# Kernel optimization log

Measured on AMD Instinct MI355X. Metric: run time of the kernel, lower is better.

## Reference

```python
import jax, jax.numpy as jnp
import numpy as np

STATE_DIM = 2
HIDDEN = 1024
N_SKILLS = 5
N_ACTIONS = 4
BATCH = 65536


def setup_inputs() -> dict:
    key = jax.random.key(0)
    ks = jax.random.split(key, 8)
    def lin_init(k, fan_in, shape):
        bound = 1.0 / np.sqrt(fan_in)
        return jax.random.uniform(k, shape, jnp.float32, -bound, bound)
    return {
        "s": jax.random.normal(ks[0], (BATCH, STATE_DIM), jnp.float32),
        "skill_idx": jax.random.randint(ks[1], (BATCH,), 0, N_SKILLS, jnp.int32),
        "W1": lin_init(ks[2], STATE_DIM, (STATE_DIM, HIDDEN)),
        "b1": lin_init(ks[3], STATE_DIM, (HIDDEN,)),
        "W2": lin_init(ks[4], HIDDEN, (HIDDEN, HIDDEN)),
        "b2": lin_init(ks[5], HIDDEN, (HIDDEN,)),
        "W_heads": lin_init(ks[6], HIDDEN, (N_SKILLS, HIDDEN, N_ACTIONS)),
        "b_heads": lin_init(ks[7], HIDDEN, (N_SKILLS, N_ACTIONS)),
    }


def reference(s, skill_idx, W1, b1, W2, b2, W_heads, b_heads):
    # shared feature MLP: Linear -> ReLU -> Linear -> ReLU
    h = jax.nn.relu(s @ W1 + b1)            # [B, H]
    feat = jax.nn.relu(h @ W2 + b2)         # [B, H]
    # per-sample skill head: gather weights then one batched contraction
    Wg = W_heads[skill_idx]                 # [B, H, A]
    bg = b_heads[skill_idx]                 # [B, A]
    return jnp.einsum('bh,bha->ba', feat, Wg) + bg  # [B, A]
```

## Files before the change

kernel.cpp:

```cpp
#include <hip/hip_runtime.h>

typedef __bf16 bf16x8 __attribute__((ext_vector_type(8)));
typedef __bf16 bf16x4 __attribute__((ext_vector_type(4)));
typedef float  floatx4 __attribute__((ext_vector_type(4)));

#define GLOBAL_AS __attribute__((address_space(1)))
#define LOCAL_AS  __attribute__((address_space(3)))

static constexpr int HID = 1024;
static constexpr int MT  = 128;
static constexpr int BK  = 64;
static constexpr int KIT = HID / BK;

__device__ __forceinline__ void h8(bf16x8& d, float s0, float s1,
                                   const float4& w0a, const float4& w0b,
                                   const float4& w1a, const float4& w1b,
                                   const float4& ba,  const float4& bb) {
    d[0] = (__bf16)fmaxf(fmaf(s1, w1a.x, fmaf(s0, w0a.x, ba.x)), 0.f);
    d[1] = (__bf16)fmaxf(fmaf(s1, w1a.y, fmaf(s0, w0a.y, ba.y)), 0.f);
    d[2] = (__bf16)fmaxf(fmaf(s1, w1a.z, fmaf(s0, w0a.z, ba.z)), 0.f);
    d[3] = (__bf16)fmaxf(fmaf(s1, w1a.w, fmaf(s0, w0a.w, ba.w)), 0.f);
    d[4] = (__bf16)fmaxf(fmaf(s1, w1b.x, fmaf(s0, w0b.x, bb.x)), 0.f);
    d[5] = (__bf16)fmaxf(fmaf(s1, w1b.y, fmaf(s0, w0b.y, bb.y)), 0.f);
    d[6] = (__bf16)fmaxf(fmaf(s1, w1b.z, fmaf(s0, w0b.z, bb.z)), 0.f);
    d[7] = (__bf16)fmaxf(fmaf(s1, w1b.w, fmaf(s0, w0b.w, bb.w)), 0.f);
}

__global__ __launch_bounds__(256)
void prep_all(const float* __restrict__ W2, const float* __restrict__ WH,
              __bf16* __restrict__ W2T, __bf16* __restrict__ WHT,
              float* __restrict__ OUT) {
    int b = blockIdx.x;
    if (b < 256) {
        ((float4*)OUT)[(size_t)b * 256 + threadIdx.x]
            = make_float4(0.f, 0.f, 0.f, 0.f);
        return;
    }
    b -= 256;
    if (b < 256) {
        __shared__ __bf16 tile[64][65];
        const int bx = b & 15;
        const int by = b >> 4;
        const int a  = threadIdx.x & 63;
        const int bb = threadIdx.x >> 6;
#pragma unroll
        for (int r = 0; r < 16; ++r) {
            const int k = r * 4 + bb;
            tile[a][k] = (__bf16)W2[(size_t)(by * 64 + k) * HID + bx * 64 + a];
        }
        __syncthreads();
#pragma unroll
        for (int r = 0; r < 16; ++r) {
            const int n = r * 4 + bb;
            const int g = a >> 3, j = a & 7;
            const int ksw = ((g ^ (n & 7)) << 3) | j;
            W2T[(size_t)(bx * 64 + n) * HID + by * 64 + ksw] = tile[n][a];
        }
    } else {
        const int r = b - 256;
        const int s = r >> 2, a = r & 3;
        for (int k = threadIdx.x; k < HID; k += 256) {
            const float v = (r < 20) ? WH[((size_t)s * HID + k) * 4 + a] : 0.f;
            const int c = k >> 7, o = (k >> 3) & 15, j = k & 7;
            const int sw = (o & 8) | ((o & 7) ^ (r & 7));
            WHT[(size_t)r * HID + c * 128 + sw * 8 + j] = (__bf16)v;
        }
    }
}

__global__ __launch_bounds__(256, 4)
void policy_main(const float* __restrict__ S,  const int* __restrict__ SK,
                 const float* __restrict__ W1, const float* __restrict__ B1,
                 const __bf16* __restrict__ W2T, const float* __restrict__ B2,
                 const __bf16* __restrict__ WHT, const float* __restrict__ BH,
                 float* __restrict__ OUT) {
    __shared__ __align__(16) char smem[40960];
    __bf16* hA    = (__bf16*)smem;
    __bf16* Bt    = (__bf16*)(smem + 16384);
    __bf16* featL = (__bf16*)smem;
    __bf16* WHTL  = (__bf16*)(smem + 32768);

    const int tid  = threadIdx.x;
    const int lane = tid & 63;
    const int wv   = tid >> 6;
    const int wm   = wv & 1;
    const int wn   = wv >> 1;
    const int l15  = lane & 15;
    const int quad = lane >> 4;
    const int n8   = blockIdx.x >> 9;
    const int i0l  = (blockIdx.x & 511) * MT;

    const int a8  = lane & 7;
    const int oct = lane >> 3;

    floatx4 acc[4][4] = {};
    floatx4 hacc[2][2] = {};

#pragma unroll
    for (int c = 0; c < 2; ++c) {
        const int rb = c * 16 + wv * 4;
        const __bf16* gp = WHT + (size_t)(rb + (lane >> 4)) * HID
                         + n8 * 128 + (lane & 15) * 8;
        __builtin_amdgcn_global_load_lds((GLOBAL_AS void*)gp,
                                         (LOCAL_AS void*)(WHTL + rb * 128), 16, 0, 0);
    }

    float2 sv[4];
#pragma unroll
    for (int k = 0; k < 4; ++k)
        sv[k] = *(const float2*)(S + (size_t)(i0l + wv * 32 + a8 + 8 * k) * 2);

#pragma unroll 1
    for (int kt = 0; kt < KIT; ++kt) {
        __syncthreads();
#pragma unroll
        for (int c = 0; c < 4; ++c) {
            const int rb = c * 32 + wv * 8;
            const __bf16* gp = W2T + (size_t)(n8 * 128 + rb + (lane >> 3)) * HID
                             + kt * BK + (lane & 7) * 8;
            __builtin_amdgcn_global_load_lds((GLOBAL_AS void*)gp,
                                             (LOCAL_AS void*)(Bt + rb * 64), 16, 0, 0);
        }
        {
            const float4 w0a = *(const float4*)(W1 + kt * BK + oct * 8);
            const float4 w0b = *(const float4*)(W1 + kt * BK + oct * 8 + 4);
            const float4 w1a = *(const float4*)(W1 + HID + kt * BK + oct * 8);
            const float4 w1b = *(const float4*)(W1 + HID + kt * BK + oct * 8 + 4);
            const float4 ba  = *(const float4*)(B1 + kt * BK + oct * 8);
            const float4 bb  = *(const float4*)(B1 + kt * BK + oct * 8 + 4);
#pragma unroll
            for (int k = 0; k < 4; ++k) {
                const int smp = wv * 32 + a8 + 8 * k;
                bf16x8 hv;
                h8(hv, sv[k].x, sv[k].y, w0a, w0b, w1a, w1b, ba, bb);
                *(bf16x8*)(hA + smp * 64 + ((oct ^ a8) << 3)) = hv;
            }
        }
        __syncthreads();
#pragma unroll
        for (int ks = 0; ks < 2; ++ks) {
            bf16x8 wf[4], hf[4];
#pragma unroll
            for (int f = 0; f < 4; ++f) {
                const int row = wn * 64 + f * 16 + l15;
                wf[f] = *(const bf16x8*)(Bt + row * 64 + (((ks * 4 + quad) ^ (row & 7)) * 8));
            }
#pragma unroll
            for (int f = 0; f < 4; ++f) {
                const int smp = wm * 64 + f * 16 + l15;
                hf[f] = *(const bf16x8*)(hA + smp * 64 + (((ks * 4 + quad) ^ (smp & 7)) * 8));
            }
#pragma unroll
            for (int fn = 0; fn < 4; ++fn)
#pragma unroll
                for (int fm = 0; fm < 4; ++fm)
                    acc[fn][fm] = __builtin_amdgcn_mfma_f32_16x16x32_bf16(
                        wf[fn], hf[fm], acc[fn][fm], 0, 0, 0);
        }
    }

    __syncthreads();
#pragma unroll
    for (int fn = 0; fn < 4; ++fn) {
        const int fcb = wn * 64 + fn * 16 + quad * 4;
        const float4 b2v = *(const float4*)(B2 + n8 * 128 + fcb);
#pragma unroll
        for (int fm = 0; fm < 4; ++fm) {
            const int smp = wm * 64 + fm * 16 + l15;
            const floatx4 v = acc[fn][fm];
            bf16x4 p;
            p[0] = (__bf16)fmaxf(v[0] + b2v.x, 0.f);
            p[1] = (__bf16)fmaxf(v[1] + b2v.y, 0.f);
            p[2] = (__bf16)fmaxf(v[2] + b2v.z, 0.f);
            p[3] = (__bf16)fmaxf(v[3] + b2v.w, 0.f);
            *(bf16x4*)(featL + smp * 128 + (((fcb >> 3) ^ (smp & 15)) << 3) + (fcb & 7)) = p;
        }
    }
    __syncthreads();

#pragma unroll
    for (int f2 = 0; f2 < 2; ++f2) {
#pragma unroll
        for (int ks2 = 0; ks2 < 4; ++ks2) {
            const int row = wv * 32 + f2 * 16 + l15;
            const bf16x8 fa = *(const bf16x8*)(featL + row * 128
                                 + (((ks2 * 4 + quad) ^ (row & 15)) << 3));
#pragma unroll
            for (int t2 = 0; t2 < 2; ++t2) {
                const int r = t2 * 16 + l15;
                const int o = ks2 * 4 + quad;
                const int sw = (o & 8) | ((o & 7) ^ (r & 7));
                const bf16x8 wb = *(const bf16x8*)(WHTL + r * 128 + sw * 8);
                hacc[f2][t2] = __builtin_amdgcn_mfma_f32_16x16x32_bf16(
                    fa, wb, hacc[f2][t2], 0, 0, 0);
            }
        }
    }

#pragma unroll
    for (int f2 = 0; f2 < 2; ++f2)
#pragma unroll
        for (int j = 0; j < 4; ++j) {
            const int smp = wv * 32 + f2 * 16 + quad * 4 + j;
            const int sk  = SK[(size_t)i0l + smp];
#pragma unroll
            for (int t2 = 0; t2 < 2; ++t2) {
                const int hc = t2 * 16 + l15;
                const int d  = hc - sk * 4;
                if (d >= 0 && d < 4) {
                    float v = hacc[f2][t2][j];
                    if (n8 == 0) v += BH[hc];
                    atomicAdd(&OUT[(size_t)(i0l + smp) * 4 + d], v);
                }
            }
        }
}

extern "C" void kernel_launch(void* const* d_in, const int* in_sizes, int n_in,
                              void* d_out, int out_size, void* d_ws, size_t ws_size,
                              hipStream_t stream) {
    const float* S  = (const float*)d_in[0];
    const int*   SK = (const int*)d_in[1];
    const float* W1 = (const float*)d_in[2];
    const float* B1 = (const float*)d_in[3];
    const float* W2 = (const float*)d_in[4];
    const float* B2 = (const float*)d_in[5];
    const float* WH = (const float*)d_in[6];
    const float* BH = (const float*)d_in[7];

    char* ws = (char*)d_ws;
    __bf16* W2T = (__bf16*)ws;
    __bf16* WHT = (__bf16*)(ws + 2 * 1024 * 1024);

    hipLaunchKernelGGL(prep_all, dim3(256 + 256 + 32), dim3(256), 0, stream,
                       W2, WH, W2T, WHT, (float*)d_out);
    hipLaunchKernelGGL(policy_main, dim3((65536 / MT) * 8), dim3(256), 0, stream,
                       S, SK, W1, B1, W2T, B2, WHT, BH, (float*)d_out);
}
```

Baseline: 229.8 us.

## Enlarge GEMM tiles to 256x256 with triple-buffered W2 loads and ping-pong h tiles

The fused MLP kernel moves from 128x128 tiles with 256 threads to 256x256 tiles with 512 threads and BK=32. W2 tiles are prefetched two steps ahead into a three-slot LDS ring. The on-the-fly ReLU(s@W1+b1) tile is double-buffered so building the next tile overlaps MFMA work, with manual waitcnt, barriers and setprio. The prep kernel now writes W2T and WHT in a k-quad-major layout that replaces the XOR swizzle. The head weights are read straight from global memory instead of being staged in LDS. Intended gains are higher arithmetic intensity, fewer blocks and fewer atomics per output, in exchange for 128KB of LDS, higher register pressure and fragile manual synchronisation.

```diff
diff --git a/kernel.cpp b/kernel.cpp
--- a/kernel.cpp
+++ b/kernel.cpp
@@ -8,9 +8,10 @@
 #define LOCAL_AS  __attribute__((address_space(3)))
 
 static constexpr int HID = 1024;
-static constexpr int MT  = 128;
-static constexpr int BK  = 64;
-static constexpr int KIT = HID / BK;
+static constexpr int BM  = 256;
+static constexpr int BN  = 256;
+static constexpr int BK  = 32;
+static constexpr int NT  = HID / BK;
 
 __device__ __forceinline__ void h8(bf16x8& d, float s0, float s1,
                                    const float4& w0a, const float4& w0b,
@@ -38,7 +39,7 @@
     }
     b -= 256;
     if (b < 256) {
-        __shared__ __bf16 tile[64][65];
+        __shared__ __align__(16) __bf16 tile[64][72];
         const int bx = b & 15;
         const int by = b >> 4;
         const int a  = threadIdx.x & 63;
@@ -49,148 +50,201 @@
             tile[a][k] = (__bf16)W2[(size_t)(by * 64 + k) * HID + bx * 64 + a];
         }
         __syncthreads();
-#pragma unroll
-        for (int r = 0; r < 16; ++r) {
-            const int n = r * 4 + bb;
-            const int g = a >> 3, j = a & 7;
-            const int ksw = ((g ^ (n & 7)) << 3) | j;
-            W2T[(size_t)(bx * 64 + n) * HID + by * 64 + ksw] = tile[n][a];
+        const int n_loc = threadIdx.x & 63;
+        const int w     = threadIdx.x >> 6;
+        const int nt    = bx >> 2;
+        const int row   = (bx & 3) * 64 + n_loc;
+#pragma unroll
+        for (int h = 0; h < 2; ++h) {
+            const int ko   = w * 2 + h;
+            const int kt   = by * 2 + (ko >> 2);
+            const int quad = ko & 3;
+            const bf16x8 v = *(const bf16x8*)&tile[n_loc][ko * 8];
+            const size_t idx = ((size_t)(nt * NT + kt) * 4 + quad) * 256 + row;
+            *(bf16x8*)(W2T + idx * 8) = v;
         }
     } else {
         const int r = b - 256;
         const int s = r >> 2, a = r & 3;
         for (int k = threadIdx.x; k < HID; k += 256) {
             const float v = (r < 20) ? WH[((size_t)s * HID + k) * 4 + a] : 0.f;
-            const int c = k >> 7, o = (k >> 3) & 15, j = k & 7;
-            const int sw = (o & 8) | ((o & 7) ^ (r & 7));
-            WHT[(size_t)r * HID + c * 128 + sw * 8 + j] = (__bf16)v;
-        }
-    }
-}
-
-__global__ __launch_bounds__(256, 4)
+            WHT[(size_t)(k >> 3) * 256 + r * 8 + (k & 7)] = (__bf16)v;
+        }
+    }
+}
+
+__global__ __launch_bounds__(512, 2)
 void policy_main(const float* __restrict__ S,  const int* __restrict__ SK,
                  const float* __restrict__ W1, const float* __restrict__ B1,
                  const __bf16* __restrict__ W2T, const float* __restrict__ B2,
                  const __bf16* __restrict__ WHT, const float* __restrict__ BH,
                  float* __restrict__ OUT) {
-    __shared__ __align__(16) char smem[40960];
-    __bf16* hA    = (__bf16*)smem;
-    __bf16* Bt    = (__bf16*)(smem + 16384);
-    __bf16* featL = (__bf16*)smem;
-    __bf16* WHTL  = (__bf16*)(smem + 32768);
+    __shared__ __align__(16) char smem[131072];
+    __bf16* A0    = (__bf16*)smem;
+    __bf16* A1    = (__bf16*)(smem + 16384);
+    __bf16* Bb    = (__bf16*)(smem + 32768);
+    __bf16* featW = (__bf16*)smem;
 
     const int tid  = threadIdx.x;
     const int lane = tid & 63;
     const int wv   = tid >> 6;
-    const int wm   = wv & 1;
-    const int wn   = wv >> 1;
     const int l15  = lane & 15;
     const int quad = lane >> 4;
-    const int n8   = blockIdx.x >> 9;
-    const int i0l  = (blockIdx.x & 511) * MT;
-
-    const int a8  = lane & 7;
-    const int oct = lane >> 3;
-
-    floatx4 acc[4][4] = {};
-    floatx4 hacc[2][2] = {};
-
-#pragma unroll
-    for (int c = 0; c < 2; ++c) {
-        const int rb = c * 16 + wv * 4;
-        const __bf16* gp = WHT + (size_t)(rb + (lane >> 4)) * HID
-                         + n8 * 128 + (lane & 15) * 8;
-        __builtin_amdgcn_global_load_lds((GLOBAL_AS void*)gp,
-                                         (LOCAL_AS void*)(WHTL + rb * 128), 16, 0, 0);
-    }
-
-    float2 sv[4];
-#pragma unroll
-    for (int k = 0; k < 4; ++k)
-        sv[k] = *(const float2*)(S + (size_t)(i0l + wv * 32 + a8 + 8 * k) * 2);
-
+    const int wm   = wv >> 2;
+    const int wn   = wv & 3;
+    const int n8   = blockIdx.x >> 8;
+    const int g    = blockIdx.x & 255;
+    const size_t i0 = (size_t)g * BM;
+
+    const int octA = wv & 3;
+    const int sgrp = wv >> 2;
+
+    floatx4 acc[8][4] = {};
+
+    float2 sv[2];
+    sv[0] = *(const float2*)(S + (i0 + sgrp * 64 + lane) * 2);
+    sv[1] = *(const float2*)(S + (i0 + 128 + sgrp * 64 + lane) * 2);
+
+    float4 w0a = *(const float4*)(W1 + octA * 8);
+    float4 w0b = *(const float4*)(W1 + octA * 8 + 4);
+    float4 w1a = *(const float4*)(W1 + HID + octA * 8);
+    float4 w1b = *(const float4*)(W1 + HID + octA * 8 + 4);
+    float4 bba = *(const float4*)(B1 + octA * 8);
+    float4 bbb = *(const float4*)(B1 + octA * 8 + 4);
+
+#pragma unroll
+    for (int t = 0; t < 2; ++t)
+#pragma unroll
+        for (int L = 0; L < 2; ++L) {
+            const int c  = wv * 2 + L;
+            const int q  = c >> 2;
+            const int r0 = (c & 3) * 64;
+            const __bf16* gp = W2T
+                + ((size_t)((n8 * NT + t) * 4 + q) * 256 + r0 + lane) * 8;
+            __builtin_amdgcn_global_load_lds((GLOBAL_AS void*)gp,
+                (LOCAL_AS void*)(Bb + t * 8192 + (q * 256 + r0) * 8), 16, 0, 0);
+        }
+
+#pragma unroll
+    for (int k = 0; k < 2; ++k) {
+        const int smp = k * 128 + sgrp * 64 + lane;
+        bf16x8 hv;
+        h8(hv, sv[k].x, sv[k].y, w0a, w0b, w1a, w1b, bba, bbb);
+        *(bf16x8*)(A0 + (octA * 256 + smp) * 8) = hv;
+    }
+    asm volatile("s_waitcnt vmcnt(2)" ::: "memory");
+    asm volatile("s_waitcnt lgkmcnt(0)" ::: "memory");
+    __builtin_amdgcn_s_barrier();
+
+    int bcur = 0, bstg = 2;
 #pragma unroll 1
-    for (int kt = 0; kt < KIT; ++kt) {
-        __syncthreads();
-#pragma unroll
-        for (int c = 0; c < 4; ++c) {
-            const int rb = c * 32 + wv * 8;
-            const __bf16* gp = W2T + (size_t)(n8 * 128 + rb + (lane >> 3)) * HID
-                             + kt * BK + (lane & 7) * 8;
-            __builtin_amdgcn_global_load_lds((GLOBAL_AS void*)gp,
-                                             (LOCAL_AS void*)(Bt + rb * 64), 16, 0, 0);
-        }
-        {
-            const float4 w0a = *(const float4*)(W1 + kt * BK + oct * 8);
-            const float4 w0b = *(const float4*)(W1 + kt * BK + oct * 8 + 4);
-            const float4 w1a = *(const float4*)(W1 + HID + kt * BK + oct * 8);
-            const float4 w1b = *(const float4*)(W1 + HID + kt * BK + oct * 8 + 4);
-            const float4 ba  = *(const float4*)(B1 + kt * BK + oct * 8);
-            const float4 bb  = *(const float4*)(B1 + kt * BK + oct * 8 + 4);
-#pragma unroll
-            for (int k = 0; k < 4; ++k) {
-                const int smp = wv * 32 + a8 + 8 * k;
+    for (int t = 0; t < NT; ++t) {
+        __bf16* Ac = (t & 1) ? A1 : A0;
+        __bf16* An = (t & 1) ? A0 : A1;
+        const __bf16* Bc = Bb + bcur * 8192;
+
+        bf16x8 wf[4], hf[4];
+#pragma unroll
+        for (int f = 0; f < 4; ++f)
+            wf[f] = *(const bf16x8*)(Bc + (quad * 256 + wn * 64 + f * 16 + l15) * 8);
+#pragma unroll
+        for (int f = 0; f < 4; ++f)
+            hf[f] = *(const bf16x8*)(Ac + (quad * 256 + wm * 128 + f * 16 + l15) * 8);
+        if (t < NT - 1) {
+            const float* wp = W1 + (t + 1) * BK + octA * 8;
+            w0a = *(const float4*)(wp);
+            w0b = *(const float4*)(wp + 4);
+            w1a = *(const float4*)(wp + HID);
+            w1b = *(const float4*)(wp + HID + 4);
+            bba = *(const float4*)(B1 + (t + 1) * BK + octA * 8);
+            bbb = *(const float4*)(B1 + (t + 1) * BK + octA * 8 + 4);
+        }
+        if (t < NT - 2) {
+#pragma unroll
+            for (int L = 0; L < 2; ++L) {
+                const int c  = wv * 2 + L;
+                const int q  = c >> 2;
+                const int r0 = (c & 3) * 64;
+                const __bf16* gp = W2T
+                    + ((size_t)((n8 * NT + (t + 2)) * 4 + q) * 256 + r0 + lane) * 8;
+                __builtin_amdgcn_global_load_lds((GLOBAL_AS void*)gp,
+                    (LOCAL_AS void*)(Bb + bstg * 8192 + (q * 256 + r0) * 8), 16, 0, 0);
+            }
+        }
+        __builtin_amdgcn_s_barrier();
+        asm volatile("s_waitcnt lgkmcnt(0)" ::: "memory");
+        __builtin_amdgcn_s_setprio(1);
+#pragma unroll
+        for (int fm = 0; fm < 4; ++fm)
+#pragma unroll
+            for (int fn = 0; fn < 4; ++fn)
+                acc[fm][fn] = __builtin_amdgcn_mfma_f32_16x16x32_bf16(
+                    wf[fn], hf[fm], acc[fm][fn], 0, 0, 0);
+        __builtin_amdgcn_s_setprio(0);
+        __builtin_amdgcn_s_barrier();
+
+        bf16x8 hf2[4];
+#pragma unroll
+        for (int f = 0; f < 4; ++f)
+            hf2[f] = *(const bf16x8*)(Ac + (quad * 256 + wm * 128 + 64 + f * 16 + l15) * 8);
+        if (t < NT - 1) {
+#pragma unroll
+            for (int k = 0; k < 2; ++k) {
+                const int smp = k * 128 + sgrp * 64 + lane;
                 bf16x8 hv;
-                h8(hv, sv[k].x, sv[k].y, w0a, w0b, w1a, w1b, ba, bb);
-                *(bf16x8*)(hA + smp * 64 + ((oct ^ a8) << 3)) = hv;
-            }
-        }
-        __syncthreads();
-#pragma unroll
-        for (int ks = 0; ks < 2; ++ks) {
-            bf16x8 wf[4], hf[4];
-#pragma unroll
-            for (int f = 0; f < 4; ++f) {
-                const int row = wn * 64 + f * 16 + l15;
-                wf[f] = *(const bf16x8*)(Bt + row * 64 + (((ks * 4 + quad) ^ (row & 7)) * 8));
-            }
-#pragma unroll
-            for (int f = 0; f < 4; ++f) {
-                const int smp = wm * 64 + f * 16 + l15;
-                hf[f] = *(const bf16x8*)(hA + smp * 64 + (((ks * 4 + quad) ^ (smp & 7)) * 8));
-            }
+                h8(hv, sv[k].x, sv[k].y, w0a, w0b, w1a, w1b, bba, bbb);
+                *(bf16x8*)(An + (octA * 256 + smp) * 8) = hv;
+            }
+        }
+        __builtin_amdgcn_s_barrier();
+        asm volatile("s_waitcnt lgkmcnt(0)" ::: "memory");
+        __builtin_amdgcn_s_setprio(1);
+#pragma unroll
+        for (int fm = 0; fm < 4; ++fm)
 #pragma unroll
             for (int fn = 0; fn < 4; ++fn)
-#pragma unroll
-                for (int fm = 0; fm < 4; ++fm)
-                    acc[fn][fm] = __builtin_amdgcn_mfma_f32_16x16x32_bf16(
-                        wf[fn], hf[fm], acc[fn][fm], 0, 0, 0);
-        }
-    }
-
-    __syncthreads();
+                acc[fm + 4][fn] = __builtin_amdgcn_mfma_f32_16x16x32_bf16(
+                    wf[fn], hf2[fm], acc[fm + 4][fn], 0, 0, 0);
+        __builtin_amdgcn_s_setprio(0);
+        asm volatile("s_waitcnt vmcnt(2)" ::: "memory");
+        __builtin_amdgcn_s_barrier();
+
+        bcur = (bcur == 2) ? 0 : bcur + 1;
+        bstg = (bstg == 2) ? 0 : bstg + 1;
+    }
+
 #pragma unroll
     for (int fn = 0; fn < 4; ++fn) {
         const int fcb = wn * 64 + fn * 16 + quad * 4;
-        const float4 b2v = *(const float4*)(B2 + n8 * 128 + fcb);
-#pragma unroll
-        for (int fm = 0; fm < 4; ++fm) {
-            const int smp = wm * 64 + fm * 16 + l15;
-            const floatx4 v = acc[fn][fm];
+        const float4 b2v = *(const float4*)(B2 + n8 * 256 + fcb);
+        const int o = fcb >> 3, j = fcb & 7;
+#pragma unroll
+        for (int fm = 0; fm < 8; ++fm) {
+            const int smp = wm * 128 + fm * 16 + l15;
+            const floatx4 v = acc[fm][fn];
             bf16x4 p;
             p[0] = (__bf16)fmaxf(v[0] + b2v.x, 0.f);
             p[1] = (__bf16)fmaxf(v[1] + b2v.y, 0.f);
             p[2] = (__bf16)fmaxf(v[2] + b2v.z, 0.f);
             p[3] = (__bf16)fmaxf(v[3] + b2v.w, 0.f);
-            *(bf16x4*)(featL + smp * 128 + (((fcb >> 3) ^ (smp & 15)) << 3) + (fcb & 7)) = p;
+            *(bf16x4*)(featW + (o * 256 + smp) * 8 + j) = p;
         }
     }
     __syncthreads();
 
+    floatx4 hacc[2][2] = {};
 #pragma unroll
     for (int f2 = 0; f2 < 2; ++f2) {
-#pragma unroll
-        for (int ks2 = 0; ks2 < 4; ++ks2) {
-            const int row = wv * 32 + f2 * 16 + l15;
-            const bf16x8 fa = *(const bf16x8*)(featL + row * 128
-                                 + (((ks2 * 4 + quad) ^ (row & 15)) << 3));
+        const int row = wv * 32 + f2 * 16 + l15;
+#pragma unroll
+        for (int ks2 = 0; ks2 < 8; ++ks2) {
+            const bf16x8 fa = *(const bf16x8*)(featW
+                                 + ((ks2 * 4 + quad) * 256 + row) * 8);
 #pragma unroll
             for (int t2 = 0; t2 < 2; ++t2) {
-                const int r = t2 * 16 + l15;
-                const int o = ks2 * 4 + quad;
-                const int sw = (o & 8) | ((o & 7) ^ (r & 7));
-                const bf16x8 wb = *(const bf16x8*)(WHTL + r * 128 + sw * 8);
+                const int r  = t2 * 16 + l15;
+                const int og = n8 * 32 + ks2 * 4 + quad;
+                const bf16x8 wb = *(const bf16x8*)(WHT + ((size_t)og * 32 + r) * 8);
                 hacc[f2][t2] = __builtin_amdgcn_mfma_f32_16x16x32_bf16(
                     fa, wb, hacc[f2][t2], 0, 0, 0);
             }
@@ -202,7 +256,7 @@
 #pragma unroll
         for (int j = 0; j < 4; ++j) {
             const int smp = wv * 32 + f2 * 16 + quad * 4 + j;
-            const int sk  = SK[(size_t)i0l + smp];
+            const int sk  = SK[i0 + smp];
 #pragma unroll
             for (int t2 = 0; t2 < 2; ++t2) {
                 const int hc = t2 * 16 + l15;
@@ -210,7 +264,7 @@
                 if (d >= 0 && d < 4) {
                     float v = hacc[f2][t2][j];
                     if (n8 == 0) v += BH[hc];
-                    atomicAdd(&OUT[(size_t)(i0l + smp) * 4 + d], v);
+                    atomicAdd(&OUT[(i0 + smp) * 4 + d], v);
                 }
             }
         }
@@ -232,8 +286,8 @@
     __bf16* W2T = (__bf16*)ws;
     __bf16* WHT = (__bf16*)(ws + 2 * 1024 * 1024);
 
-    hipLaunchKernelGGL(prep_all, dim3(256 + 256 + 32), dim3(256), 0, stream,
+    hipLaunchKernelGGL(prep_all, dim3(544), dim3(256), 0, stream,
                        W2, WH, W2T, WHT, (float*)d_out);
-    hipLaunchKernelGGL(policy_main, dim3((65536 / MT) * 8), dim3(256), 0, stream,
+    hipLaunchKernelGGL(policy_main, dim3(1024), dim3(512), 0, stream,
                        S, SK, W1, B1, W2T, B2, WHT, BH, (float*)d_out);
 }
```

Result: slower. 263.2 us (+14.5%).

## Retile main GEMM to 64 samples x 256 features with MFMA-fragment weight layout

Applied to the files above, without the earlier changes.

Changes the block tile from 128 samples x 128 output features to 64 samples x 256 features. Each wave now owns 64 feature columns, so only 4 feature slabs (and 4 atomic partial sums per output) are produced instead of 8. W2 and the head weights are pre-laid out in MFMA fragment order so LDS and global loads are linear and need no XOR swizzle. Head weights are read straight from global memory instead of being staged in LDS. In exchange the per-block W2 tile doubles while the recomputed layer-1 activations per block halve, and the occupancy hint drops from 4 to 3 blocks.

```diff
diff --git a/kernel.cpp b/kernel.cpp
--- a/kernel.cpp
+++ b/kernel.cpp
@@ -8,7 +8,6 @@
 #define LOCAL_AS  __attribute__((address_space(3)))
 
 static constexpr int HID = 1024;
-static constexpr int MT  = 128;
 static constexpr int BK  = 64;
 static constexpr int KIT = HID / BK;
 
@@ -38,7 +37,7 @@
     }
     b -= 256;
     if (b < 256) {
-        __shared__ __bf16 tile[64][65];
+        __shared__ __align__(16) __bf16 tile[64][72];
         const int bx = b & 15;
         const int by = b >> 4;
         const int a  = threadIdx.x & 63;
@@ -49,107 +48,91 @@
             tile[a][k] = (__bf16)W2[(size_t)(by * 64 + k) * HID + bx * 64 + a];
         }
         __syncthreads();
-#pragma unroll
-        for (int r = 0; r < 16; ++r) {
-            const int n = r * 4 + bb;
-            const int g = a >> 3, j = a & 7;
-            const int ksw = ((g ^ (n & 7)) << 3) | j;
-            W2T[(size_t)(bx * 64 + n) * HID + by * 64 + ksw] = tile[n][a];
+        const int slab = bx >> 2;
+#pragma unroll
+        for (int p = 0; p < 2; ++p) {
+            const int idx = p * 256 + threadIdx.x;
+            const int c   = idx & 63;
+            const int oct = idx >> 6;
+            const bf16x8 v = *(const bf16x8*)&tile[c][oct * 8];
+            const int col = (bx & 3) * 64 + c;
+            const size_t dst = ((size_t)(slab * KIT + by) * 8 + oct) * 256 + col;
+            *(bf16x8*)(W2T + dst * 8) = v;
         }
     } else {
         const int r = b - 256;
         const int s = r >> 2, a = r & 3;
         for (int k = threadIdx.x; k < HID; k += 256) {
             const float v = (r < 20) ? WH[((size_t)s * HID + k) * 4 + a] : 0.f;
-            const int c = k >> 7, o = (k >> 3) & 15, j = k & 7;
-            const int sw = (o & 8) | ((o & 7) ^ (r & 7));
-            WHT[(size_t)r * HID + c * 128 + sw * 8 + j] = (__bf16)v;
-        }
-    }
-}
-
-__global__ __launch_bounds__(256, 4)
+            WHT[(size_t)(k >> 3) * 256 + r * 8 + (k & 7)] = (__bf16)v;
+        }
+    }
+}
+
+__global__ __launch_bounds__(256, 3)
 void policy_main(const float* __restrict__ S,  const int* __restrict__ SK,
                  const float* __restrict__ W1, const float* __restrict__ B1,
                  const __bf16* __restrict__ W2T, const float* __restrict__ B2,
                  const __bf16* __restrict__ WHT, const float* __restrict__ BH,
                  float* __restrict__ OUT) {
     __shared__ __align__(16) char smem[40960];
-    __bf16* hA    = (__bf16*)smem;
-    __bf16* Bt    = (__bf16*)(smem + 16384);
-    __bf16* featL = (__bf16*)smem;
-    __bf16* WHTL  = (__bf16*)(smem + 32768);
+    __bf16* At    = (__bf16*)smem;
+    __bf16* Bt    = (__bf16*)(smem + 8192);
+    __bf16* featL = (__bf16*)(smem + 8192);
 
     const int tid  = threadIdx.x;
     const int lane = tid & 63;
     const int wv   = tid >> 6;
-    const int wm   = wv & 1;
-    const int wn   = wv >> 1;
     const int l15  = lane & 15;
     const int quad = lane >> 4;
-    const int n8   = blockIdx.x >> 9;
-    const int i0l  = (blockIdx.x & 511) * MT;
-
-    const int a8  = lane & 7;
-    const int oct = lane >> 3;
+    const int slab = blockIdx.x >> 10;
+    const int g    = blockIdx.x & 1023;
+    const size_t i0 = (size_t)g * 64;
+
+    const int octA = wv * 2 + (lane >> 5);
+    const int smpA = lane & 31;
 
     floatx4 acc[4][4] = {};
-    floatx4 hacc[2][2] = {};
-
-#pragma unroll
-    for (int c = 0; c < 2; ++c) {
-        const int rb = c * 16 + wv * 4;
-        const __bf16* gp = WHT + (size_t)(rb + (lane >> 4)) * HID
-                         + n8 * 128 + (lane & 15) * 8;
-        __builtin_amdgcn_global_load_lds((GLOBAL_AS void*)gp,
-                                         (LOCAL_AS void*)(WHTL + rb * 128), 16, 0, 0);
-    }
-
-    float2 sv[4];
-#pragma unroll
-    for (int k = 0; k < 4; ++k)
-        sv[k] = *(const float2*)(S + (size_t)(i0l + wv * 32 + a8 + 8 * k) * 2);
+
+    const float2 sv0 = *(const float2*)(S + (i0 + smpA) * 2);
+    const float2 sv1 = *(const float2*)(S + (i0 + 32 + smpA) * 2);
 
 #pragma unroll 1
     for (int kt = 0; kt < KIT; ++kt) {
         __syncthreads();
 #pragma unroll
-        for (int c = 0; c < 4; ++c) {
-            const int rb = c * 32 + wv * 8;
-            const __bf16* gp = W2T + (size_t)(n8 * 128 + rb + (lane >> 3)) * HID
-                             + kt * BK + (lane & 7) * 8;
+        for (int L = 0; L < 8; ++L) {
+            const __bf16* gp = W2T
+                + (((size_t)(slab * KIT + kt) * 8 + L) * 256 + wv * 64 + lane) * 8;
             __builtin_amdgcn_global_load_lds((GLOBAL_AS void*)gp,
-                                             (LOCAL_AS void*)(Bt + rb * 64), 16, 0, 0);
+                (LOCAL_AS void*)(Bt + (L * 256 + wv * 64) * 8), 16, 0, 0);
         }
         {
-            const float4 w0a = *(const float4*)(W1 + kt * BK + oct * 8);
-            const float4 w0b = *(const float4*)(W1 + kt * BK + oct * 8 + 4);
-            const float4 w1a = *(const float4*)(W1 + HID + kt * BK + oct * 8);
-            const float4 w1b = *(const float4*)(W1 + HID + kt * BK + oct * 8 + 4);
-            const float4 ba  = *(const float4*)(B1 + kt * BK + oct * 8);
-            const float4 bb  = *(const float4*)(B1 + kt * BK + oct * 8 + 4);
-#pragma unroll
-            for (int k = 0; k < 4; ++k) {
-                const int smp = wv * 32 + a8 + 8 * k;
-                bf16x8 hv;
-                h8(hv, sv[k].x, sv[k].y, w0a, w0b, w1a, w1b, ba, bb);
-                *(bf16x8*)(hA + smp * 64 + ((oct ^ a8) << 3)) = hv;
-            }
+            const float* wp = W1 + kt * BK + octA * 8;
+            const float4 w0a = *(const float4*)(wp);
+            const float4 w0b = *(const float4*)(wp + 4);
+            const float4 w1a = *(const float4*)(wp + HID);
+            const float4 w1b = *(const float4*)(wp + HID + 4);
+            const float4 ba  = *(const float4*)(B1 + kt * BK + octA * 8);
+            const float4 bb  = *(const float4*)(B1 + kt * BK + octA * 8 + 4);
+            bf16x8 hv;
+            h8(hv, sv0.x, sv0.y, w0a, w0b, w1a, w1b, ba, bb);
+            *(bf16x8*)(At + (octA * 64 + smpA) * 8) = hv;
+            h8(hv, sv1.x, sv1.y, w0a, w0b, w1a, w1b, ba, bb);
+            *(bf16x8*)(At + (octA * 64 + 32 + smpA) * 8) = hv;
         }
         __syncthreads();
 #pragma unroll
         for (int ks = 0; ks < 2; ++ks) {
             bf16x8 wf[4], hf[4];
 #pragma unroll
-            for (int f = 0; f < 4; ++f) {
-                const int row = wn * 64 + f * 16 + l15;
-                wf[f] = *(const bf16x8*)(Bt + row * 64 + (((ks * 4 + quad) ^ (row & 7)) * 8));
-            }
-#pragma unroll
-            for (int f = 0; f < 4; ++f) {
-                const int smp = wm * 64 + f * 16 + l15;
-                hf[f] = *(const bf16x8*)(hA + smp * 64 + (((ks * 4 + quad) ^ (smp & 7)) * 8));
-            }
+            for (int f = 0; f < 4; ++f)
+                wf[f] = *(const bf16x8*)(Bt
+                         + (((ks * 4 + quad) * 256) + wv * 64 + f * 16 + l15) * 8);
+#pragma unroll
+            for (int f = 0; f < 4; ++f)
+                hf[f] = *(const bf16x8*)(At
+                         + (((ks * 4 + quad) * 64) + f * 16 + l15) * 8);
 #pragma unroll
             for (int fn = 0; fn < 4; ++fn)
 #pragma unroll
@@ -162,58 +145,53 @@
     __syncthreads();
 #pragma unroll
     for (int fn = 0; fn < 4; ++fn) {
-        const int fcb = wn * 64 + fn * 16 + quad * 4;
-        const float4 b2v = *(const float4*)(B2 + n8 * 128 + fcb);
+        const int fcb = wv * 64 + fn * 16 + quad * 4;
+        const float4 b2v = *(const float4*)(B2 + slab * 256 + fcb);
+        const int o = fcb >> 3, j = fcb & 7;
 #pragma unroll
         for (int fm = 0; fm < 4; ++fm) {
-            const int smp = wm * 64 + fm * 16 + l15;
+            const int smp = fm * 16 + l15;
             const floatx4 v = acc[fn][fm];
             bf16x4 p;
             p[0] = (__bf16)fmaxf(v[0] + b2v.x, 0.f);
             p[1] = (__bf16)fmaxf(v[1] + b2v.y, 0.f);
             p[2] = (__bf16)fmaxf(v[2] + b2v.z, 0.f);
             p[3] = (__bf16)fmaxf(v[3] + b2v.w, 0.f);
-            *(bf16x4*)(featL + smp * 128 + (((fcb >> 3) ^ (smp & 15)) << 3) + (fcb & 7)) = p;
+            *(bf16x4*)(featL + (o * 64 + smp) * 8 + j) = p;
         }
     }
     __syncthreads();
 
-#pragma unroll
-    for (int f2 = 0; f2 < 2; ++f2) {
-#pragma unroll
-        for (int ks2 = 0; ks2 < 4; ++ks2) {
-            const int row = wv * 32 + f2 * 16 + l15;
-            const bf16x8 fa = *(const bf16x8*)(featL + row * 128
-                                 + (((ks2 * 4 + quad) ^ (row & 15)) << 3));
-#pragma unroll
-            for (int t2 = 0; t2 < 2; ++t2) {
-                const int r = t2 * 16 + l15;
-                const int o = ks2 * 4 + quad;
-                const int sw = (o & 8) | ((o & 7) ^ (r & 7));
-                const bf16x8 wb = *(const bf16x8*)(WHTL + r * 128 + sw * 8);
-                hacc[f2][t2] = __builtin_amdgcn_mfma_f32_16x16x32_bf16(
-                    fa, wb, hacc[f2][t2], 0, 0, 0);
+    floatx4 hacc[2] = {};
+#pragma unroll
+    for (int ks2 = 0; ks2 < 8; ++ks2) {
+        const bf16x8 fa = *(const bf16x8*)(featL
+                             + ((ks2 * 4 + quad) * 64 + wv * 16 + l15) * 8);
+#pragma unroll
+        for (int t2 = 0; t2 < 2; ++t2) {
+            const int r  = t2 * 16 + l15;
+            const int og = slab * 32 + ks2 * 4 + quad;
+            const bf16x8 wb = *(const bf16x8*)(WHT + (size_t)og * 256 + r * 8);
+            hacc[t2] = __builtin_amdgcn_mfma_f32_16x16x32_bf16(
+                fa, wb, hacc[t2], 0, 0, 0);
+        }
+    }
+
+#pragma unroll
+    for (int j = 0; j < 4; ++j) {
+        const int smp = wv * 16 + quad * 4 + j;
+        const int sk  = SK[i0 + smp];
+#pragma unroll
+        for (int t2 = 0; t2 < 2; ++t2) {
+            const int hc = t2 * 16 + l15;
+            const int d  = hc - sk * 4;
+            if (d >= 0 && d < 4) {
+                float v = hacc[t2][j];
+                if (slab == 0) v += BH[hc];
+                atomicAdd(&OUT[(i0 + smp) * 4 + d], v);
             }
         }
     }
-
-#pragma unroll
-    for (int f2 = 0; f2 < 2; ++f2)
-#pragma unroll
-        for (int j = 0; j < 4; ++j) {
-            const int smp = wv * 32 + f2 * 16 + quad * 4 + j;
-            const int sk  = SK[(size_t)i0l + smp];
-#pragma unroll
-            for (int t2 = 0; t2 < 2; ++t2) {
-                const int hc = t2 * 16 + l15;
-                const int d  = hc - sk * 4;
-                if (d >= 0 && d < 4) {
-                    float v = hacc[f2][t2][j];
-                    if (n8 == 0) v += BH[hc];
-                    atomicAdd(&OUT[(size_t)(i0l + smp) * 4 + d], v);
-                }
-            }
-        }
 }
 
 extern "C" void kernel_launch(void* const* d_in, const int* in_sizes, int n_in,
@@ -232,8 +210,8 @@
     __bf16* W2T = (__bf16*)ws;
     __bf16* WHT = (__bf16*)(ws + 2 * 1024 * 1024);
 
-    hipLaunchKernelGGL(prep_all, dim3(256 + 256 + 32), dim3(256), 0, stream,
+    hipLaunchKernelGGL(prep_all, dim3(544), dim3(256), 0, stream,
                        W2, WH, W2T, WHT, (float*)d_out);
-    hipLaunchKernelGGL(policy_main, dim3((65536 / MT) * 8), dim3(256), 0, stream,
+    hipLaunchKernelGGL(policy_main, dim3(4096), dim3(256), 0, stream,
                        S, SK, W1, B1, W2T, B2, WHT, BH, (float*)d_out);
 }
```

Result: faster. 224.8 us (-2.2%).
